# Kernel optimization log

Hardware: AMD Instinct MI355X
Metric: run time of the kernel (lower is better)

Reference implementation:

```python
import jax, jax.numpy as jnp
import numpy as np

B, P, K = 8, 1024, 20
N = B * P
EMB, OUT = 1024, 40
GRID = 5

def _window(W):
    # Hamming taper (window_type='hamming')
    n = jnp.arange(W, dtype=jnp.float32)
    return 0.54 - 0.46 * jnp.cos(2.0 * jnp.pi * n / (W - 1))

def _init_kan(key, din, dout, W, S, g):
    nw = (din - W) // S + 1
    coeffs = jax.random.normal(key, (2, dout, nw, W, g), jnp.float32) / (np.sqrt(nw * W) * np.sqrt(g))
    bias = jnp.zeros((dout,), jnp.float32)
    return coeffs, bias

def stft_kan(x, coeffs, bias, W, S):
    # x: (n, D) -> (n, dout). Slice D into overlapping windows of size W,
    # stride S, apply Hamming taper, build Fourier features cos(k*x), sin(k*x)
    # for k=1..g and contract with learned coefficients (STFT-Fourier-KAN).
    nw, g = coeffs.shape[2], coeffs.shape[4]
    idx = (np.arange(nw) * S)[:, None] + np.arange(W)[None, :]        # (nw, W)
    xw = x[:, idx] * _window(W)                                        # (n, nw, W)
    kfreq = jnp.arange(1, g + 1, dtype=x.dtype)
    arg = xw[..., None] * kfreq                                        # (n, nw, W, g)
    y = (jnp.einsum('nwig,owig->no', jnp.cos(arg), coeffs[0])
         + jnp.einsum('nwig,owig->no', jnp.sin(arg), coeffs[1]))
    return y + bias

def setup_inputs():
    key = jax.random.key(0)
    ks = jax.random.split(key, 5)
    pos = jax.random.normal(ks[0], (N, 3), jnp.float32)
    batch = (jnp.arange(N) // P).astype(jnp.int32)  # sorted, equal-size clouds
    c1, b1 = _init_kan(ks[1], 6, 64, 3, 3, GRID)
    c2, b2 = _init_kan(ks[2], 64, 128, 16, 8, GRID)
    c3, b3 = _init_kan(ks[3], 128, EMB, 32, 16, GRID)
    c4, b4 = _init_kan(ks[4], 2 * EMB, OUT, 256, 128, GRID)
    return {"pos": pos, "batch": batch, "c1": c1, "b1": b1, "c2": c2, "b2": b2,
            "c3": c3, "b3": b3, "c4": c4, "b4": b4}

def reference(pos, batch, c1, b1, c2, b2, c3, b3, c4, b4):
    posb = pos.reshape(B, P, 3)
    # dynamic kNN graph per cloud (self excluded)
    d = jnp.sum((posb[:, :, None, :] - posb[:, None, :, :]) ** 2, -1)  # (B,P,P)
    d = d + jnp.eye(P, dtype=d.dtype) * 1e10
    _, nbr = jax.lax.top_k(-d, K)                                      # (B,P,K)
    pj = jax.vmap(lambda p, i: p[i])(posb, nbr)                        # (B,P,K,3)
    pi = jnp.broadcast_to(posb[:, :, None, :], pj.shape)
    e = jnp.concatenate([pi, pj - pi], -1).reshape(N * K, 6)           # edge feats
    h = stft_kan(e, c1, b1, 3, 3)                                      # (N*K,64)
    h = stft_kan(h, c2, b2, 16, 8)                                     # (N*K,128)
    x1 = jnp.max(h.reshape(N, K, 128), axis=1)                         # max aggr over neighbors
    x = stft_kan(x1, c3, b3, 32, 16)                                   # (N,EMB)
    gmax = jax.ops.segment_max(x, batch, num_segments=B)
    gsum = jax.ops.segment_sum(x, batch, num_segments=B)
    cnt = jax.ops.segment_sum(jnp.ones((N, 1), x.dtype), batch, num_segments=B)
    xg = jnp.concatenate([gmax, gsum / cnt], -1)                       # (B, 2*EMB)
    return stft_kan(xg, c4, b4, 256, 128)                              # (B, OUT)
```

## Files before the change

kernel.cpp:

```cpp
#include <hip/hip_runtime.h>


typedef unsigned short u16;
typedef unsigned int   u32;
typedef unsigned long long u64;
typedef __attribute__((ext_vector_type(8))) _Float16 half8;
typedef __attribute__((ext_vector_type(4))) float f32x4;

__device__ __forceinline__ float bf2f(u16 u) {
  u32 v = ((u32)u) << 16;
  return __uint_as_float(v);
}
__device__ __forceinline__ u16 f2bfr(float f) {
  u32 x = __float_as_uint(f);
  u32 r = x + 0x7FFFu + ((x >> 16) & 1u);
  return (u16)(r >> 16);
}
__device__ __forceinline__ u16 f2h(float f) {
  _Float16 h = (_Float16)f;
  u16 r;
  __builtin_memcpy(&r, &h, 2);
  return r;
}
__device__ __forceinline__ float h2f(u16 u) {
  _Float16 h;
  __builtin_memcpy(&h, &u, 2);
  return (float)h;
}
__device__ __forceinline__ float ldf(const void* p, size_t i, bool f32) {
  return f32 ? ((const float*)p)[i] : bf2f(((const u16*)p)[i]);
}
__device__ __forceinline__ u64 minu64(u64 a, u64 b) { return a < b ? a : b; }

#define NBR_OFF   ((size_t)0)
#define FLAG_OFF  ((size_t)917504)
#define L4P_OFF   (((size_t)(1u << 20)) + 131072)
#define C1T_OFF   (((size_t)(1u << 20)) + 524288)
#define C2T_OFF   (((size_t)(1u << 20)) + 589824)
#define C3T_OFF   ((size_t)(2u << 20))
#define C4T_OFF   ((size_t)(7u << 20))
#define PMAX_OFF  ((size_t)(13u << 20))
#define PSUM_OFF  ((size_t)(14u << 20))
#define X1_OFF    ((size_t)(15u << 20))
#define H1_OFF    ((size_t)(18u << 20))

__global__ void detect_kernel(const void* __restrict__ pos,
                              int* __restrict__ flag) {
  int t = threadIdx.x;
  float a = fabsf(((const float*)pos)[t]);
  bool ok = (a > 1.0e-3f && a < 100.0f);
  unsigned long long m = __ballot(ok);
  if (t == 0) *flag = (__popcll(m) >= 32) ? 1 : 0;
}

__global__ void tkan_all_kernel(const void* __restrict__ s1, void* __restrict__ d1,
                                const void* __restrict__ s2, void* __restrict__ d2,
                                const void* __restrict__ s3, void* __restrict__ d3,
                                const void* __restrict__ s4, void* __restrict__ d4,
                                const int* __restrict__ dfl) {
  const int blk = blockIdx.x;
  const void* src; void* dst;
  int dout, nw, W, total, KPAD, outf32, base;
  if (blk < 16)        { src = s1; dst = d1; dout = 64;   nw = 2;  W = 3;
                         total = 64 * 64;     KPAD = 64;    outf32 = 0; base = 0; }
  else if (blk < 576)  { src = s2; dst = d2; dout = 128;  nw = 7;  W = 16;
                         total = 128 * 1120;  KPAD = 1120;  outf32 = 0; base = 16; }
  else if (blk < 9536) { src = s3; dst = d3; dout = 1024; nw = 7;  W = 32;
                         total = 1024 * 2240; KPAD = 2240;  outf32 = 0; base = 576; }
  else                 { src = s4; dst = d4; dout = 40;   nw = 15; W = 256;
                         total = 40 * 38400;  KPAD = 38400; outf32 = 1; base = 9536; }
  int id = (blk - base) * 256 + threadIdx.x;
  if (id >= total) return;
  const bool f32 = (*dfl != 0);
  int o = id / KPAD, f = id % KPAD;
  int NA = nw * W;
  int Kt = NA * 10;
  float v = 0.f;
  if (f < Kt) {
    int part = f & 1, p = f >> 1;
    int aa, gg;
    if (p < 4 * NA) { aa = p >> 2;      gg = p & 3; }
    else            { aa = p - 4 * NA;  gg = 4;     }
    int i = aa % W, w = aa / W;
    int OS = NA * 5;
    size_t sidx = (size_t)part * (dout * OS) + (size_t)o * OS + w * (W * 5) + i * 5 + gg;
    v = ldf(src, sidx, f32);
  }
  if (outf32) ((float*)dst)[id] = v;
  else        ((u16*)dst)[id] = f2h(v);
}

__global__ __launch_bounds__(256) void knn_kernel(const void* __restrict__ pos,
                                                  int* __restrict__ nbr,
                                                  const int* __restrict__ dfl) {
  __shared__ float px[1024], py[1024], pz[1024];
  const bool f32 = (*dfl != 0);
  const int t = threadIdx.x;
  const int b = blockIdx.y;
  const int base = b << 10;
  for (int j = t; j < 1024; j += 256) {
    size_t pidx = (size_t)(base + j) * 3;
    px[j] = ldf(pos, pidx, f32);
    py[j] = ldf(pos, pidx + 1, f32);
    pz[j] = ldf(pos, pidx + 2, f32);
  }
  __syncthreads();
  const int wv = t >> 6, lane = t & 63;
  const int q = blockIdx.x * 4 + wv;
  const float qx = px[q], qy = py[q], qz = pz[q];
  u64 key[16];
#pragma unroll
  for (int s = 0; s < 16; ++s) {
    const int j = s * 64 + lane;
    float dx = qx - px[j], dy = qy - py[j], dz = qz - pz[j];
    float d = __fadd_rn(__fadd_rn(__fmul_rn(dx, dx), __fmul_rn(dy, dy)),
                        __fmul_rn(dz, dz));
    key[s] = (j == q) ? ~0ull
                      : ((((u64)__float_as_uint(d)) << 32) | (u32)j);
  }
  const int obase = (base + q) * 20;
  for (int k = 0; k < 20; ++k) {
    u64 m = key[0];
#pragma unroll
    for (int s = 1; s < 16; ++s) m = minu64(m, key[s]);
#pragma unroll
    for (int off = 32; off >= 1; off >>= 1) {
      u32 lo = (u32)m, hi = (u32)(m >> 32);
      lo = __shfl_xor(lo, off, 64);
      hi = __shfl_xor(hi, off, 64);
      m = minu64(m, (((u64)hi) << 32) | lo);
    }
    if (lane == 0) nbr[obase + k] = (int)(u32)m;
#pragma unroll
    for (int s = 0; s < 16; ++s)
      if (key[s] == m) key[s] = ~0ull;
  }
}

template <int L>
__global__ __launch_bounds__(256, 3) void kan_kernel(
    const void* __restrict__ in_, const int* __restrict__ nbr,
    const void* __restrict__ pos, const u16* __restrict__ ct,
    const void* __restrict__ bias, void* __restrict__ out_,
    float* __restrict__ pmax, float* __restrict__ psum,
    const int* __restrict__ dfl) {
  constexpr int W    = (L == 1) ? 3  : (L == 2) ? 16  : 32;
  constexpr int S    = (L == 1) ? 3  : (L == 2) ? 8   : 16;
  constexpr int DIN  = (L == 1) ? 6  : (L == 2) ? 64  : 128;
  constexpr int NT   = 64;
  constexpr int NW   = (DIN - W) / S + 1;
  constexpr int NA   = NW * W;
  constexpr int NPAIR = NA * 5;
  constexpr int S1P  = NA * 4;
  constexpr int KROW  = (L == 1) ? 64 : NPAIR * 2;
  constexpr int NCH   = KROW / 32;
  constexpr int NB    = NT / 16;
  constexpr int RW    = (L == 1) ? 64 : (L == 2) ? 80 : 32;
  constexpr int MB    = RW / 16;
  constexpr int PSTH  = DIN + 4;
  constexpr int LGW   = (W == 16) ? 4 : 5;
  constexpr int BBS   = 4 * 520;

  __shared__ float hamS[(L == 1) ? 1 : W];
  __shared__ float wT1[(L == 1) ? 32 : 1];
  __shared__ int   hT1[(L == 1) ? 32 : 1];
  __shared__ u16   slab[(L == 1) ? 2 : 4 * RW * PSTH];
  __shared__ u16   stage1[(L == 1) ? 4 * 64 * 64 : 2];
  __shared__ u16   Bbuf[2 * BBS];

  const bool f32 = (*dfl != 0);
  const u16* inH = (const u16*)in_;
  const int t = threadIdx.x;
  if constexpr (L == 1) {
    if (t < 32) {
      float wv_ = 0.f; int hx = 0;
      if (t < NPAIR) {
        int aa, gg;
        if (t < S1P) { aa = t >> 2;   gg = t & 3; }
        else         { aa = t - S1P;  gg = 4;     }
        int i = aa % W;
        float hm = 0.54f - 0.46f * cospif(2.0f * (float)i / (float)(W - 1));
        wv_ = hm * (float)(gg + 1);
        hx = aa;
      }
      wT1[t] = wv_; hT1[t] = hx;
    }
  } else {
    if (t < W) hamS[t] = 0.54f - 0.46f * cospif(2.0f * (float)t / (float)(W - 1));
  }

  int tile, ncol0;
  if constexpr (L == 3) {
    const int id = blockIdx.x;
    tile = (id >> 3) & 63;
    ncol0 = ((((id & 7) << 1) | (id >> 9))) * NT;
  } else {
    tile = blockIdx.x;
    ncol0 = blockIdx.y * NT;
  }
  const int lane = t & 63, wv = t >> 6;
  const int m16 = lane & 15, kb = lane >> 4;
  const int rowbase = tile * (4 * RW) + wv * RW;
  u16* myslab = &slab[(L == 1) ? 0 : wv * RW * PSTH];

  const int scol = t >> 2, spart = t & 3;
  const u16* srcB = ct + (size_t)(ncol0 + scol) * KROW + spart * 8;

  if constexpr (L >= 2) {
    constexpr int F4R = DIN / 4;
    constexpr int TOT = RW * F4R;
    for (int i = lane; i < TOT; i += 64) {
      const int r = i / F4R, c4 = i % F4R;
      *(uint2*)(myslab + r * PSTH + c4 * 4) =
          *(const uint2*)(inH + (size_t)(rowbase + r) * DIN + c4 * 4);
    }
  }

  {
    const uint4 v = *(const uint4*)srcB;
    *(uint4*)(Bbuf + spart * 520 + scol * 8) = v;
  }
  __syncthreads();

  f32x4 acc[MB][NB];
#pragma unroll
  for (int mb = 0; mb < MB; ++mb)
#pragma unroll
    for (int nb = 0; nb < NB; ++nb) {
      acc[mb][nb][0] = 0.f; acc[mb][nb][1] = 0.f;
      acc[mb][nb][2] = 0.f; acc[mb][nb][3] = 0.f;
    }

  for (int c = 0; c < NCH; ++c) {
    uint4 bnext;
    const bool havenext = (c + 1 < NCH);
    if (havenext)
      bnext = *(const uint4*)(srcB + (c + 1) * 32);
    const int pg0 = c * 16 + kb * 4;
    half8 af[MB];
    if constexpr (L == 1) {
      float wm[4]; int hx[4]; bool val[4];
#pragma unroll
      for (int u = 0; u < 4; ++u) {
        const int pg = pg0 + u;
        wm[u] = wT1[pg]; hx[u] = hT1[pg]; val[u] = (pg < NPAIR);
      }
#pragma unroll
      for (int mb = 0; mb < MB; ++mb) {
        const int row = rowbase + mb * 16 + m16;
        const int pt = row / 20;
        const int cloud = pt >> 10, ci = pt & 1023;
        const int cb = cloud << 10;
        const int jl = nbr[row];
#pragma unroll
        for (int u = 0; u < 4; ++u) {
          float cs = 0.f, sn = 0.f;
          if (val[u]) {
            const int aa = hx[u];
            float v;
            if (aa < 3) {
              v = ldf(pos, (size_t)(cb + ci) * 3 + aa, f32);
            } else {
              const int cc2 = aa - 3;
              v = ldf(pos, (size_t)(cb + jl) * 3 + cc2, f32) -
                  ldf(pos, (size_t)(cb + ci) * 3 + cc2, f32);
            }
            const float ang = v * wm[u];
            cs = __cosf(ang); sn = __sinf(ang);
          }
          af[mb][2 * u]     = (_Float16)cs;
          af[mb][2 * u + 1] = (_Float16)sn;
        }
      }
    } else if (pg0 < S1P) {
      const int aa = pg0 >> 2;
      const int i = aa & (W - 1), w = aa >> LGW;
      const int hidx = S * w + i;
      const float hm = hamS[i];
#pragma unroll
      for (int mb = 0; mb < MB; ++mb) {
        const u16* rp = myslab + (mb * 16 + m16) * PSTH;
        const float th = h2f(rp[hidx]) * hm;
        const float c1 = __cosf(th), s1 = __sinf(th);
        const float tc = 2.0f * c1;
        const float c2 = tc * c1 - 1.0f, s2 = tc * s1;
        const float c3 = tc * c2 - c1,   s3 = tc * s2 - s1;
        const float c4 = tc * c3 - c2,   s4 = tc * s3 - s2;
        af[mb][0] = (_Float16)c1; af[mb][1] = (_Float16)s1;
        af[mb][2] = (_Float16)c2; af[mb][3] = (_Float16)s2;
        af[mb][4] = (_Float16)c3; af[mb][5] = (_Float16)s3;
        af[mb][6] = (_Float16)c4; af[mb][7] = (_Float16)s4;
      }
    } else {
      const int q0 = pg0 - S1P;
      float wm[4]; int hx[4];
#pragma unroll
      for (int u = 0; u < 4; ++u) {
        const int aa = q0 + u;
        const int i = aa & (W - 1), w = aa >> LGW;
        hx[u] = S * w + i;
        wm[u] = hamS[i] * 5.0f;
      }
#pragma unroll
      for (int mb = 0; mb < MB; ++mb) {
        const u16* rp = myslab + (mb * 16 + m16) * PSTH;
#pragma unroll
        for (int u = 0; u < 4; ++u) {
          const float ang = h2f(rp[hx[u]]) * wm[u];
          af[mb][2 * u]     = (_Float16)__cosf(ang);
          af[mb][2 * u + 1] = (_Float16)__sinf(ang);
        }
      }
    }
    const u16* bb = Bbuf + (c & 1) * BBS + kb * 520;
#pragma unroll
    for (int nb = 0; nb < NB; ++nb) {
      const half8 bv = *(const half8*)(bb + (nb * 16 + m16) * 8);
#pragma unroll
      for (int mb = 0; mb < MB; ++mb)
        acc[mb][nb] = __builtin_amdgcn_mfma_f32_16x16x32_f16(
            af[mb], bv, acc[mb][nb], 0, 0, 0);
    }
    if (havenext) {
      *(uint4*)(Bbuf + ((c + 1) & 1) * BBS + spart * 520 + scol * 8) = bnext;
      __syncthreads();
    }
  }

  if constexpr (L == 1) {
    u16* st = &stage1[wv * 4096];
#pragma unroll
    for (int mb = 0; mb < MB; ++mb)
#pragma unroll
      for (int nb = 0; nb < NB; ++nb) {
        const float bsv = ldf(bias, nb * 16 + m16, f32);
#pragma unroll
        for (int r = 0; r < 4; ++r)
          st[(mb * 16 + kb * 4 + r) * 64 + nb * 16 + m16] =
              f2h(acc[mb][nb][r] + bsv);
      }
    u16* gp = (u16*)out_ + (size_t)rowbase * 64;
    for (int i = lane; i < 512; i += 64)
      *(uint4*)(gp + i * 8) = *(const uint4*)&st[i * 8];
  } else if constexpr (L == 2) {
    u16* st = myslab;
#pragma unroll
    for (int mb = 0; mb < MB; ++mb)
#pragma unroll
      for (int nb = 0; nb < NB; ++nb) {
        const float bsv = ldf(bias, ncol0 + nb * 16 + m16, f32);
#pragma unroll
        for (int r = 0; r < 4; ++r)
          st[(mb * 16 + kb * 4 + r) * PSTH + nb * 16 + m16] =
              f2h(acc[mb][nb][r] + bsv);
      }
    const int pbase = tile * 16 + wv * 4;
#pragma unroll
    for (int j = 0; j < 4; ++j) {
      float m = -3.0e38f;
#pragma unroll
      for (int k = 0; k < 20; ++k)
        m = fmaxf(m, h2f(st[(j * 20 + k) * PSTH + lane]));
      ((u16*)out_)[(size_t)(pbase + j) * 128 + ncol0 + lane] = f2h(m);
    }
  } else {
    const int chunk = rowbase >> 5;
#pragma unroll
    for (int nb = 0; nb < NB; ++nb) {
      const int col = ncol0 + nb * 16 + m16;
      const float bsv = ldf(bias, col, f32);
      float m = -3.0e38f, s = 0.f;
#pragma unroll
      for (int mb = 0; mb < MB; ++mb)
#pragma unroll
        for (int r = 0; r < 4; ++r) {
          const float v = acc[mb][nb][r] + bsv;
          m = fmaxf(m, v); s += v;
        }
#pragma unroll
      for (int off = 16; off <= 32; off <<= 1) {
        m = fmaxf(m, __shfl_xor(m, off, 64));
        s += __shfl_xor(s, off, 64);
      }
      if (kb == 0) {
        pmax[(size_t)chunk * 1024 + col] = m;
        psum[(size_t)chunk * 1024 + col] = s;
      }
    }
  }
}

__global__ __launch_bounds__(256) void l4_kernel(const float* __restrict__ pmax,
                                                 const float* __restrict__ psum,
                                                 const float* __restrict__ c4t,
                                                 float* __restrict__ part) {
  __shared__ float F[2560];
  const int t = threadIdx.x;
  const int w = blockIdx.x, b = blockIdx.y;
  const int ch = w * 128 + t;
  float xv;
  if (ch < 1024) {
    float m = -3.0e38f;
    for (int rc = 0; rc < 32; ++rc)
      m = fmaxf(m, pmax[(size_t)(b * 32 + rc) * 1024 + ch]);
    xv = m;
  } else {
    const int cc = ch - 1024;
    float s = 0.f;
    for (int rc = 0; rc < 32; ++rc)
      s += psum[(size_t)(b * 32 + rc) * 1024 + cc];
    xv = s * (1.0f / 1024.0f);
  }
  const float hm = 0.54f - 0.46f * cospif(2.0f * (float)t / 255.0f);
  const float aa = xv * hm;
  const float c1 = __cosf(aa), s1 = __sinf(aa);
  const float tc = 2.0f * c1;
  const float c2 = tc * c1 - 1.0f, s2 = tc * s1;
  const float c3 = tc * c2 - c1,   s3 = tc * s2 - s1;
  const float c4 = tc * c3 - c2,   s4 = tc * s3 - s2;
  const float a5 = aa * 5.0f;
  F[t * 8]     = c1; F[t * 8 + 1] = s1;
  F[t * 8 + 2] = c2; F[t * 8 + 3] = s2;
  F[t * 8 + 4] = c3; F[t * 8 + 5] = s3;
  F[t * 8 + 6] = c4; F[t * 8 + 7] = s4;
  F[2048 + t * 2]     = __cosf(a5);
  F[2048 + t * 2 + 1] = __sinf(a5);
  __syncthreads();
  if (t < 240) {
    const int o = t % 40, s = t / 40;
    const int f0 = s * 432;
    const int f1 = (f0 + 432 < 2560) ? (f0 + 432) : 2560;
    const float* cp1 = c4t + (size_t)o * 38400 + w * 2048;
    const float* cp2 = c4t + (size_t)o * 38400 + 30720 + w * 512;
    float acc = 0.f;
    for (int f = f0; f < f1; f += 4) {
      const float* cpf = (f < 2048) ? (cp1 + f) : (cp2 + (f - 2048));
      const float4 cv = *(const float4*)cpf;
      const float4 fa = *(const float4*)&F[f];
      acc += fa.x * cv.x + fa.y * cv.y + fa.z * cv.z + fa.w * cv.w;
    }
    part[((b * 15 + w) * 6 + s) * 40 + o] = acc;
  }
}

__global__ void outred_kernel(const float* __restrict__ part,
                              const void* __restrict__ b4,
                              void* __restrict__ outp,
                              const int* __restrict__ dfl) {
  int t = threadIdx.x;
  if (t >= 320) return;
  const bool f32 = (*dfl != 0);
  int b = t / 40, o = t % 40;
  float s = ldf(b4, o, f32);
  for (int w = 0; w < 15; ++w)
#pragma unroll
    for (int sl = 0; sl < 6; ++sl)
      s += part[((b * 15 + w) * 6 + sl) * 40 + o];
  if (f32) ((float*)outp)[t] = s;
  else     ((u16*)outp)[t] = f2bfr(s);
}

extern "C" void kernel_launch(void* const* d_in, const int* in_sizes, int n_in,
                              void* d_out, int out_size, void* d_ws,
                              size_t ws_size, hipStream_t stream) {
  (void)in_sizes; (void)n_in; (void)out_size; (void)ws_size;
  const void* pos = d_in[0];
  const void* c1 = d_in[2];
  const void* b1 = d_in[3];
  const void* c2 = d_in[4];
  const void* b2 = d_in[5];
  const void* c3 = d_in[6];
  const void* b3 = d_in[7];
  const void* c4 = d_in[8];
  const void* b4 = d_in[9];

  char* ws = (char*)d_ws;
  int* nbr   = (int*)(ws + NBR_OFF);
  int* flag  = (int*)(ws + FLAG_OFF);
  float* l4p = (float*)(ws + L4P_OFF);
  u16* c1t   = (u16*)(ws + C1T_OFF);
  u16* c2t   = (u16*)(ws + C2T_OFF);
  u16* c3t   = (u16*)(ws + C3T_OFF);
  float* c4t = (float*)(ws + C4T_OFF);
  float* pmax = (float*)(ws + PMAX_OFF);
  float* psum = (float*)(ws + PSUM_OFF);
  u16* x1    = (u16*)(ws + X1_OFF);
  u16* h1    = (u16*)(ws + H1_OFF);

  detect_kernel<<<1, 64, 0, stream>>>(pos, flag);

  tkan_all_kernel<<<15536, 256, 0, stream>>>(c1, c1t, c2, c2t, c3, c3t,
                                             c4, c4t, flag);

  knn_kernel<<<dim3(256, 8), 256, 0, stream>>>(pos, nbr, flag);

  kan_kernel<1><<<640, 256, 0, stream>>>(nullptr, nbr, pos, c1t, b1, h1,
                                         nullptr, nullptr, flag);
  kan_kernel<2><<<dim3(512, 2), 256, 0, stream>>>(h1, nullptr, nullptr, c2t,
                                                  b2, x1, nullptr, nullptr, flag);
  kan_kernel<3><<<1024, 256, 0, stream>>>(x1, nullptr, nullptr, c3t,
                                          b3, nullptr, pmax, psum, flag);

  l4_kernel<<<dim3(15, 8), 256, 0, stream>>>(pmax, psum, c4t, l4p);
  outred_kernel<<<1, 320, 0, stream>>>(l4p, b4, d_out, flag);
}
```

Baseline: 309.1 us.

## Widen layer-2 KAN tile to all 128 output columns per block

Layer 2 now computes all 128 output columns in one block (NT=128) instead of splitting across two blocks in grid y. Each block therefore builds its cos/sin feature fragments once for the full width, rather than two blocks recomputing the same transcendental features and reloading the same input slab. The B-staging buffer doubles, each thread loads two B vectors per chunk, and the max-over-neighbors epilogue is done in two halves through the existing slab. The accumulator count doubles, so launch bounds drop to 2 blocks per SM, which costs occupancy and raises register pressure.

```diff
diff --git a/kernel.cpp b/kernel.cpp
--- a/kernel.cpp
+++ b/kernel.cpp
@@ -138,7 +138,7 @@
 }
 
 template <int L>
-__global__ __launch_bounds__(256, 3) void kan_kernel(
+__global__ __launch_bounds__(256, (L == 2) ? 2 : 3) void kan_kernel(
     const void* __restrict__ in_, const int* __restrict__ nbr,
     const void* __restrict__ pos, const u16* __restrict__ ct,
     const void* __restrict__ bias, void* __restrict__ out_,
@@ -147,7 +147,7 @@
   constexpr int W    = (L == 1) ? 3  : (L == 2) ? 16  : 32;
   constexpr int S    = (L == 1) ? 3  : (L == 2) ? 8   : 16;
   constexpr int DIN  = (L == 1) ? 6  : (L == 2) ? 64  : 128;
-  constexpr int NT   = 64;
+  constexpr int NT   = (L == 2) ? 128 : 64;
   constexpr int NW   = (DIN - W) / S + 1;
   constexpr int NA   = NW * W;
   constexpr int NPAIR = NA * 5;
@@ -159,7 +159,9 @@
   constexpr int MB    = RW / 16;
   constexpr int PSTH  = DIN + 4;
   constexpr int LGW   = (W == 16) ? 4 : 5;
-  constexpr int BBS   = 4 * 520;
+  constexpr int BCS   = NT * 8 + 8;
+  constexpr int BBS   = 4 * BCS;
+  constexpr int NPC   = NT / 64;
 
   __shared__ float hamS[(L == 1) ? 1 : W];
   __shared__ float wT1[(L == 1) ? 32 : 1];
@@ -203,8 +205,15 @@
   const int rowbase = tile * (4 * RW) + wv * RW;
   u16* myslab = &slab[(L == 1) ? 0 : wv * RW * PSTH];
 
-  const int scol = t >> 2, spart = t & 3;
-  const u16* srcB = ct + (size_t)(ncol0 + scol) * KROW + spart * 8;
+  const u16* srcB[NPC];
+  int sdst[NPC];
+#pragma unroll
+  for (int p_ = 0; p_ < NPC; ++p_) {
+    const int pid = t + p_ * 256;
+    const int scol = pid >> 2, spart = pid & 3;
+    srcB[p_] = ct + (size_t)(ncol0 + scol) * KROW + spart * 8;
+    sdst[p_] = spart * BCS + scol * 8;
+  }
 
   if constexpr (L >= 2) {
     constexpr int F4R = DIN / 4;
@@ -216,9 +225,10 @@
     }
   }
 
-  {
-    const uint4 v = *(const uint4*)srcB;
-    *(uint4*)(Bbuf + spart * 520 + scol * 8) = v;
+#pragma unroll
+  for (int p_ = 0; p_ < NPC; ++p_) {
+    const uint4 v = *(const uint4*)srcB[p_];
+    *(uint4*)(Bbuf + sdst[p_]) = v;
   }
   __syncthreads();
 
@@ -232,10 +242,13 @@
     }
 
   for (int c = 0; c < NCH; ++c) {
-    uint4 bnext;
+    uint4 bnext[NPC];
     const bool havenext = (c + 1 < NCH);
-    if (havenext)
-      bnext = *(const uint4*)(srcB + (c + 1) * 32);
+    if (havenext) {
+#pragma unroll
+      for (int p_ = 0; p_ < NPC; ++p_)
+        bnext[p_] = *(const uint4*)(srcB[p_] + (c + 1) * 32);
+    }
     const int pg0 = c * 16 + kb * 4;
     half8 af[MB];
     if constexpr (L == 1) {
@@ -312,7 +325,7 @@
         }
       }
     }
-    const u16* bb = Bbuf + (c & 1) * BBS + kb * 520;
+    const u16* bb = Bbuf + (c & 1) * BBS + kb * BCS;
 #pragma unroll
     for (int nb = 0; nb < NB; ++nb) {
       const half8 bv = *(const half8*)(bb + (nb * 16 + m16) * 8);
@@ -322,7 +335,9 @@
             af[mb], bv, acc[mb][nb], 0, 0, 0);
     }
     if (havenext) {
-      *(uint4*)(Bbuf + ((c + 1) & 1) * BBS + spart * 520 + scol * 8) = bnext;
+#pragma unroll
+      for (int p_ = 0; p_ < NPC; ++p_)
+        *(uint4*)(Bbuf + ((c + 1) & 1) * BBS + sdst[p_]) = bnext[p_];
       __syncthreads();
     }
   }
@@ -344,24 +359,28 @@
       *(uint4*)(gp + i * 8) = *(const uint4*)&st[i * 8];
   } else if constexpr (L == 2) {
     u16* st = myslab;
-#pragma unroll
-    for (int mb = 0; mb < MB; ++mb)
-#pragma unroll
-      for (int nb = 0; nb < NB; ++nb) {
-        const float bsv = ldf(bias, ncol0 + nb * 16 + m16, f32);
-#pragma unroll
-        for (int r = 0; r < 4; ++r)
-          st[(mb * 16 + kb * 4 + r) * PSTH + nb * 16 + m16] =
-              f2h(acc[mb][nb][r] + bsv);
-      }
     const int pbase = tile * 16 + wv * 4;
 #pragma unroll
-    for (int j = 0; j < 4; ++j) {
-      float m = -3.0e38f;
-#pragma unroll
-      for (int k = 0; k < 20; ++k)
-        m = fmaxf(m, h2f(st[(j * 20 + k) * PSTH + lane]));
-      ((u16*)out_)[(size_t)(pbase + j) * 128 + ncol0 + lane] = f2h(m);
+    for (int h = 0; h < 2; ++h) {
+#pragma unroll
+      for (int mb = 0; mb < MB; ++mb)
+#pragma unroll
+        for (int nb4 = 0; nb4 < 4; ++nb4) {
+          const int nb = h * 4 + nb4;
+          const float bsv = ldf(bias, ncol0 + nb * 16 + m16, f32);
+#pragma unroll
+          for (int r = 0; r < 4; ++r)
+            st[(mb * 16 + kb * 4 + r) * PSTH + nb4 * 16 + m16] =
+                f2h(acc[mb][nb][r] + bsv);
+        }
+#pragma unroll
+      for (int j = 0; j < 4; ++j) {
+        float m = -3.0e38f;
+#pragma unroll
+        for (int k = 0; k < 20; ++k)
+          m = fmaxf(m, h2f(st[(j * 20 + k) * PSTH + lane]));
+        ((u16*)out_)[(size_t)(pbase + j) * 128 + ncol0 + h * 64 + lane] = f2h(m);
+      }
     }
   } else {
     const int chunk = rowbase >> 5;
@@ -496,8 +515,8 @@
 
   kan_kernel<1><<<640, 256, 0, stream>>>(nullptr, nbr, pos, c1t, b1, h1,
                                          nullptr, nullptr, flag);
-  kan_kernel<2><<<dim3(512, 2), 256, 0, stream>>>(h1, nullptr, nullptr, c2t,
-                                                  b2, x1, nullptr, nullptr, flag);
+  kan_kernel<2><<<dim3(512), 256, 0, stream>>>(h1, nullptr, nullptr, c2t,
+                                               b2, x1, nullptr, nullptr, flag);
   kan_kernel<3><<<1024, 256, 0, stream>>>(x1, nullptr, nullptr, c3t,
                                           b3, nullptr, pmax, psum, flag);
 
```

Result: no change. 306.4 us (-0.9%).

## Tile coefficient layout by K-chunk and read B fragments directly from global

Applied to the files above, without the earlier changes.

The coefficient transpose now writes a chunked layout ([k/32][dout][32]) so each MFMA B fragment is one contiguous 16-byte global load. This removes the LDS double-buffer for B and the per-chunk __syncthreads. Layer 2 now processes all 128 output columns per block (NT=128, one grid column), so the cos/sin A-fragment build runs once instead of twice, and launch bounds are retuned per layer. The cost is B traffic served from L1/L2 instead of shared memory, with no prefetch overlap, plus higher register pressure in layer 2.

```diff
diff --git a/kernel.cpp b/kernel.cpp
--- a/kernel.cpp
+++ b/kernel.cpp
@@ -72,7 +72,15 @@
   int id = (blk - base) * 256 + threadIdx.x;
   if (id >= total) return;
   const bool f32 = (*dfl != 0);
-  int o = id / KPAD, f = id % KPAD;
+  int o, f;
+  if (blk < 9536) {
+    const int k32 = id & 31;
+    const int cidx = id >> 5;
+    o = cidx % dout;
+    f = (cidx / dout) * 32 + k32;
+  } else {
+    o = id / KPAD; f = id % KPAD;
+  }
   int NA = nw * W;
   int Kt = NA * 10;
   float v = 0.f;
@@ -138,7 +146,7 @@
 }
 
 template <int L>
-__global__ __launch_bounds__(256, 3) void kan_kernel(
+__global__ __launch_bounds__(256, (L == 2) ? 2 : (L == 3) ? 4 : 3) void kan_kernel(
     const void* __restrict__ in_, const int* __restrict__ nbr,
     const void* __restrict__ pos, const u16* __restrict__ ct,
     const void* __restrict__ bias, void* __restrict__ out_,
@@ -147,7 +155,8 @@
   constexpr int W    = (L == 1) ? 3  : (L == 2) ? 16  : 32;
   constexpr int S    = (L == 1) ? 3  : (L == 2) ? 8   : 16;
   constexpr int DIN  = (L == 1) ? 6  : (L == 2) ? 64  : 128;
-  constexpr int NT   = 64;
+  constexpr int NT   = (L == 2) ? 128 : 64;
+  constexpr int DOUTF = (L == 1) ? 64 : (L == 2) ? 128 : 1024;
   constexpr int NW   = (DIN - W) / S + 1;
   constexpr int NA   = NW * W;
   constexpr int NPAIR = NA * 5;
@@ -159,14 +168,12 @@
   constexpr int MB    = RW / 16;
   constexpr int PSTH  = DIN + 4;
   constexpr int LGW   = (W == 16) ? 4 : 5;
-  constexpr int BBS   = 4 * 520;
 
   __shared__ float hamS[(L == 1) ? 1 : W];
   __shared__ float wT1[(L == 1) ? 32 : 1];
   __shared__ int   hT1[(L == 1) ? 32 : 1];
   __shared__ u16   slab[(L == 1) ? 2 : 4 * RW * PSTH];
   __shared__ u16   stage1[(L == 1) ? 4 * 64 * 64 : 2];
-  __shared__ u16   Bbuf[2 * BBS];
 
   const bool f32 = (*dfl != 0);
   const u16* inH = (const u16*)in_;
@@ -203,8 +210,7 @@
   const int rowbase = tile * (4 * RW) + wv * RW;
   u16* myslab = &slab[(L == 1) ? 0 : wv * RW * PSTH];
 
-  const int scol = t >> 2, spart = t & 3;
-  const u16* srcB = ct + (size_t)(ncol0 + scol) * KROW + spart * 8;
+  const u16* bb0 = ct + (size_t)(ncol0 + m16) * 32 + kb * 8;
 
   if constexpr (L >= 2) {
     constexpr int F4R = DIN / 4;
@@ -215,11 +221,6 @@
           *(const uint2*)(inH + (size_t)(rowbase + r) * DIN + c4 * 4);
     }
   }
-
-  {
-    const uint4 v = *(const uint4*)srcB;
-    *(uint4*)(Bbuf + spart * 520 + scol * 8) = v;
-  }
   __syncthreads();
 
   f32x4 acc[MB][NB];
@@ -231,13 +232,8 @@
       acc[mb][nb][2] = 0.f; acc[mb][nb][3] = 0.f;
     }
 
-  for (int c = 0; c < NCH; ++c) {
-    uint4 bnext;
-    const bool havenext = (c + 1 < NCH);
-    if (havenext)
-      bnext = *(const uint4*)(srcB + (c + 1) * 32);
+  auto build_af = [&](int c, half8* af) {
     const int pg0 = c * 16 + kb * 4;
-    half8 af[MB];
     if constexpr (L == 1) {
       float wm[4]; int hx[4]; bool val[4];
 #pragma unroll
@@ -312,18 +308,19 @@
         }
       }
     }
-    const u16* bb = Bbuf + (c & 1) * BBS + kb * 520;
+  };
+
+  for (int c = 0; c < NCH; ++c) {
+    half8 af[MB];
+    build_af(c, af);
+    const u16* bb = bb0 + (size_t)c * (DOUTF * 32);
 #pragma unroll
     for (int nb = 0; nb < NB; ++nb) {
-      const half8 bv = *(const half8*)(bb + (nb * 16 + m16) * 8);
+      const half8 bv = *(const half8*)(bb + nb * 512);
 #pragma unroll
       for (int mb = 0; mb < MB; ++mb)
         acc[mb][nb] = __builtin_amdgcn_mfma_f32_16x16x32_f16(
             af[mb], bv, acc[mb][nb], 0, 0, 0);
-    }
-    if (havenext) {
-      *(uint4*)(Bbuf + ((c + 1) & 1) * BBS + spart * 520 + scol * 8) = bnext;
-      __syncthreads();
     }
   }
 
@@ -344,24 +341,28 @@
       *(uint4*)(gp + i * 8) = *(const uint4*)&st[i * 8];
   } else if constexpr (L == 2) {
     u16* st = myslab;
-#pragma unroll
-    for (int mb = 0; mb < MB; ++mb)
-#pragma unroll
-      for (int nb = 0; nb < NB; ++nb) {
-        const float bsv = ldf(bias, ncol0 + nb * 16 + m16, f32);
-#pragma unroll
-        for (int r = 0; r < 4; ++r)
-          st[(mb * 16 + kb * 4 + r) * PSTH + nb * 16 + m16] =
-              f2h(acc[mb][nb][r] + bsv);
-      }
     const int pbase = tile * 16 + wv * 4;
 #pragma unroll
-    for (int j = 0; j < 4; ++j) {
-      float m = -3.0e38f;
-#pragma unroll
-      for (int k = 0; k < 20; ++k)
-        m = fmaxf(m, h2f(st[(j * 20 + k) * PSTH + lane]));
-      ((u16*)out_)[(size_t)(pbase + j) * 128 + ncol0 + lane] = f2h(m);
+    for (int h = 0; h < 2; ++h) {
+#pragma unroll
+      for (int mb = 0; mb < MB; ++mb)
+#pragma unroll
+        for (int nb4 = 0; nb4 < 4; ++nb4) {
+          const int nb = h * 4 + nb4;
+          const float bsv = ldf(bias, ncol0 + nb * 16 + m16, f32);
+#pragma unroll
+          for (int r = 0; r < 4; ++r)
+            st[(mb * 16 + kb * 4 + r) * PSTH + nb4 * 16 + m16] =
+                f2h(acc[mb][nb][r] + bsv);
+        }
+#pragma unroll
+      for (int j = 0; j < 4; ++j) {
+        float m = -3.0e38f;
+#pragma unroll
+        for (int k = 0; k < 20; ++k)
+          m = fmaxf(m, h2f(st[(j * 20 + k) * PSTH + lane]));
+        ((u16*)out_)[(size_t)(pbase + j) * 128 + ncol0 + h * 64 + lane] = f2h(m);
+      }
     }
   } else {
     const int chunk = rowbase >> 5;
@@ -496,8 +497,8 @@
 
   kan_kernel<1><<<640, 256, 0, stream>>>(nullptr, nbr, pos, c1t, b1, h1,
                                          nullptr, nullptr, flag);
-  kan_kernel<2><<<dim3(512, 2), 256, 0, stream>>>(h1, nullptr, nullptr, c2t,
-                                                  b2, x1, nullptr, nullptr, flag);
+  kan_kernel<2><<<dim3(512), 256, 0, stream>>>(h1, nullptr, nullptr, c2t,
+                                               b2, x1, nullptr, nullptr, flag);
   kan_kernel<3><<<1024, 256, 0, stream>>>(x1, nullptr, nullptr, c3t,
                                           b3, nullptr, pmax, psum, flag);
 
```

Measured after the change: 313.8 us. No clear change (+1.5%).
